# Optimization experiments

Hardware: AMD Instinct MI355X
Metric: run time of the kernel (lower is better)

## Reference

```python
import jax, jax.numpy as jnp
import numpy as np

HEADS = 4
DIM_HEAD = 32
EPS = 1e-5

def _layernorm(x, g, b):
    mu = jnp.mean(x, axis=-1, keepdims=True)
    var = jnp.var(x, axis=-1, keepdims=True)
    return (x - mu) * jax.lax.rsqrt(var + EPS) * g + b

def setup_inputs() -> dict:
    key = jax.random.key(0)
    ks = jax.random.split(key, 8)
    B, C, H, W = 16, 256, 32, 32
    N = H * W
    inner = HEADS * DIM_HEAD  # 128
    s = lambda d: 1.0 / np.sqrt(d)
    return {
        "x": jax.random.normal(ks[0], (B, C, H, W), jnp.float32),
        "pos_embedding": jax.random.normal(ks[1], (1, N, C), jnp.float32),
        "w_qkv": jax.random.normal(ks[2], (C, inner * 3), jnp.float32) * s(C),
        "w_out": jax.random.normal(ks[3], (inner, C), jnp.float32) * s(inner),
        "b_out": jnp.zeros((C,), jnp.float32),
        "w_ff1": jax.random.normal(ks[4], (C, inner), jnp.float32) * s(C),
        "b_ff1": jnp.zeros((inner,), jnp.float32),
        "w_ff2": jax.random.normal(ks[5], (inner, C), jnp.float32) * s(inner),
        "b_ff2": jnp.zeros((C,), jnp.float32),
        "g1": jnp.ones((C,), jnp.float32),
        "beta1": jnp.zeros((C,), jnp.float32),
        "g2": jnp.ones((C,), jnp.float32),
        "beta2": jnp.zeros((C,), jnp.float32),
    }

def reference(x, pos_embedding, w_qkv, w_out, b_out, w_ff1, b_ff1, w_ff2, b_ff2, g1, beta1, g2, beta2):
    b, c, h, w = x.shape
    n = h * w
    tok = jnp.transpose(x.reshape(b, c, n), (0, 2, 1))  # [b, n, c]
    tok = tok + pos_embedding  # (dropout is identity at eval)
    # attention
    qkv = _layernorm(tok, g1, beta1) @ w_qkv  # [b, n, 3*inner]
    qkv = qkv.reshape(b, n, 3, HEADS, DIM_HEAD)
    q, k, v = qkv[:, :, 0], qkv[:, :, 1], qkv[:, :, 2]  # [b, n, h, d]
    scale = DIM_HEAD ** -0.5
    dots = jnp.einsum('bihd,bjhd->bhij', q, k) * scale
    attn = jax.nn.softmax(dots, axis=-1)
    out = jnp.einsum('bhij,bjhd->bihd', attn, v).reshape(b, n, HEADS * DIM_HEAD)
    tok = out @ w_out + b_out + tok
    # ffn
    hdn = jax.nn.gelu(_layernorm(tok, g2, beta2) @ w_ff1 + b_ff1, approximate=False)
    tok = hdn @ w_ff2 + b_ff2 + tok
    return jnp.transpose(tok, (0, 2, 1)).reshape(b, c, h, w)
```

## Files before the change

### kernel.cpp

```cpp
#include <hip/hip_runtime.h>
#include <hip/hip_bf16.h>
#include <math.h>

#define B_     16
#define C_     256
#define N_     1024
#define HEADS_ 4
#define DH_    32
#define INNER_ 128
#define EPS_   1e-5f

typedef __attribute__((ext_vector_type(8))) short bf16x8;
typedef __attribute__((ext_vector_type(4))) float f32x4;

__device__ __forceinline__ ushort f2bf(float f) {
  union { float f; unsigned u; } v; v.f = f;
  unsigned u = v.u;
  return (ushort)((u + 0x7fffu + ((u >> 16) & 1u)) >> 16);
}
__device__ __forceinline__ float bf2f(ushort u) {
  union { unsigned u; float f; } v; v.u = ((unsigned)u) << 16;
  return v.f;
}
__device__ __forceinline__ unsigned cvt_pk_bf16(float lo, float hi) {
  unsigned r;
  asm("v_cvt_pk_bf16_f32 %0, %1, %2" : "=v"(r) : "v"(lo), "v"(hi));
  return r;
}

#define QSCALE_ 0.2550348652979437f

__global__ __launch_bounds__(256) void k_wconv(
    const float* __restrict__ wqkv, const float* __restrict__ wout,
    const float* __restrict__ wff1, const float* __restrict__ wff2,
    ushort* __restrict__ wqkvT, ushort* __restrict__ woutT,
    ushort* __restrict__ wff1T, ushort* __restrict__ wff2T) {
  int i = blockIdx.x * 256 + threadIdx.x;
  if (i < 98304) {
    int k = i / 384, n = i % 384;
    wqkvT[n * 256 + k] = f2bf(wqkv[i]);
    return;
  }
  i -= 98304;
  if (i < 32768) {
    int k = i / 256, n = i % 256;
    woutT[n * 128 + k] = f2bf(wout[i]);
    return;
  }
  i -= 32768;
  if (i < 32768) {
    int k = i / 128, n = i % 128;
    wff1T[n * 256 + k] = f2bf(wff1[i]);
    return;
  }
  i -= 32768;
  {
    int k = i / 256, n = i % 256;
    wff2T[n * 128 + k] = f2bf(wff2[i]);
  }
}

__global__ __launch_bounds__(256) void k_pos_ln(
    const float* __restrict__ x, const float* __restrict__ pos,
    const float* __restrict__ g1, const float* __restrict__ beta1,
    ushort* __restrict__ tokb, ushort* __restrict__ xn) {
  const int b  = blockIdx.x >> 4;
  const int n0 = (blockIdx.x & 15) << 6;
  const int t  = threadIdx.x;
  __shared__ float xs[C_][68];
  {
    const int cq = t >> 4, nq = t & 15;
#pragma unroll
    for (int i = 0; i < 16; ++i) {
      const int c = i * 16 + cq;
      const float4 v = *reinterpret_cast<const float4*>(
          &x[((size_t)b * C_ + c) * N_ + n0 + 4 * nq]);
      *reinterpret_cast<float4*>(&xs[c][4 * nq]) = v;
    }
  }
  __syncthreads();
  const int tl = t >> 2, sub = t & 3, c0 = sub * 64;
  const int n = n0 + tl;
  float v[64];
#pragma unroll
  for (int i = 0; i < 64; ++i) v[i] = xs[c0 + i][tl];
#pragma unroll
  for (int j = 0; j < 16; ++j) {
    const float4 p = *reinterpret_cast<const float4*>(&pos[(size_t)n * C_ + c0 + 4 * j]);
    v[4*j] += p.x; v[4*j+1] += p.y; v[4*j+2] += p.z; v[4*j+3] += p.w;
  }
  float s = 0.f;
#pragma unroll
  for (int i = 0; i < 64; ++i) s += v[i];
  s += __shfl_xor(s, 1); s += __shfl_xor(s, 2);
  const float mu = s * (1.f / C_);
  float sq = 0.f;
#pragma unroll
  for (int i = 0; i < 64; ++i) { const float d = v[i] - mu; sq += d * d; }
  sq += __shfl_xor(sq, 1); sq += __shfl_xor(sq, 2);
  const float rs = rsqrtf(sq * (1.f / C_) + EPS_);
  ushort* tokrow = &tokb[((size_t)b * N_ + n) * C_ + c0];
  ushort* xnrow  = &xn[((size_t)b * N_ + n) * C_ + c0];
#pragma unroll
  for (int j = 0; j < 16; ++j) {
    ushort4 tu;
    tu.x = f2bf(v[4*j]);   tu.y = f2bf(v[4*j+1]);
    tu.z = f2bf(v[4*j+2]); tu.w = f2bf(v[4*j+3]);
    *reinterpret_cast<ushort4*>(&tokrow[4 * j]) = tu;
    const float4 g  = *reinterpret_cast<const float4*>(&g1[c0 + 4 * j]);
    const float4 be = *reinterpret_cast<const float4*>(&beta1[c0 + 4 * j]);
    ushort4 u;
    u.x = f2bf((v[4*j]   - mu) * rs * g.x + be.x);
    u.y = f2bf((v[4*j+1] - mu) * rs * g.y + be.y);
    u.z = f2bf((v[4*j+2] - mu) * rs * g.z + be.z);
    u.w = f2bf((v[4*j+3] - mu) * rs * g.w + be.w);
    *reinterpret_cast<ushort4*>(&xnrow[4 * j]) = u;
  }
}

__global__ __launch_bounds__(256) void k_qkv(
    const ushort* __restrict__ xn, const ushort* __restrict__ wqkvT,
    ushort* __restrict__ qb, ushort* __restrict__ kb, ushort* __restrict__ vtb) {
  const int T0 = blockIdx.x * 32;
  const int w = threadIdx.x >> 6, lane = threadIdx.x & 63;
  const int li = lane & 15, g = lane >> 4;

  bf16x8 Bf[2][8];
#pragma unroll
  for (int nf = 0; nf < 2; ++nf)
#pragma unroll
    for (int ks = 0; ks < 8; ++ks)
      Bf[nf][ks] = *reinterpret_cast<const bf16x8*>(
          &xn[((size_t)(T0 + nf * 16 + li)) * C_ + ks * 32 + 8 * g]);

#pragma unroll
  for (int mf = 0; mf < 6; ++mf) {
    const int chb = w * 96 + mf * 16;
    bf16x8 Af[8];
#pragma unroll
    for (int ks = 0; ks < 8; ++ks)
      Af[ks] = *reinterpret_cast<const bf16x8*>(
          &wqkvT[(size_t)(chb + li) * C_ + ks * 32 + 8 * g]);
#pragma unroll
    for (int nf = 0; nf < 2; ++nf) {
      f32x4 acc = {0.f, 0.f, 0.f, 0.f};
#pragma unroll
      for (int ks = 0; ks < 8; ++ks)
        acc = __builtin_amdgcn_mfma_f32_16x16x32_bf16(Af[ks], Bf[nf][ks], acc, 0, 0, 0);
      const int tokg = T0 + nf * 16 + li;
      const int bb = tokg >> 10, nn = tokg & 1023;
      const int ch0 = chb + 4 * g;
      if (ch0 < 128) {
        const int h = ch0 >> 5, dh = ch0 & 31;
        ushort4 u;
        u.x = f2bf(acc[0] * QSCALE_); u.y = f2bf(acc[1] * QSCALE_);
        u.z = f2bf(acc[2] * QSCALE_); u.w = f2bf(acc[3] * QSCALE_);
        *reinterpret_cast<ushort4*>(&qb[(((size_t)(bb * HEADS_ + h)) * N_ + nn) * DH_ + dh]) = u;
      } else if (ch0 < 256) {
        const int c2 = ch0 - 128, h = c2 >> 5, dh = c2 & 31;
        ushort4 u;
        u.x = f2bf(acc[0]); u.y = f2bf(acc[1]); u.z = f2bf(acc[2]); u.w = f2bf(acc[3]);
        *reinterpret_cast<ushort4*>(&kb[(((size_t)(bb * HEADS_ + h)) * N_ + nn) * DH_ + dh]) = u;
      } else {
        const int c2 = ch0 - 256, h = c2 >> 5, dh = c2 & 31;
        ushort* base = &vtb[(((size_t)(bb * HEADS_ + h)) * DH_ + dh) * N_ + nn];
        base[0] = f2bf(acc[0]); base[N_] = f2bf(acc[1]);
        base[2 * N_] = f2bf(acc[2]); base[3 * N_] = f2bf(acc[3]);
      }
    }
  }
}

__global__ __launch_bounds__(256) void k_attn(
    const ushort* __restrict__ qb, const ushort* __restrict__ kb,
    const ushort* __restrict__ vtb, ushort* __restrict__ ao) {
  const int blk = blockIdx.x;
  const int b   = blk >> 5;
  const int h   = (blk >> 3) & 3;
  const int qt2 = blk & 7;
  const int tid = threadIdx.x;
  const int w = tid >> 6, lane = tid & 63;
  const int qi = lane & 15, g = lane >> 4;

  __shared__ __align__(16) ushort P_lds[4][2][16][80];

  const int bh  = b * HEADS_ + h;
  const int nq0 = qt2 * 128 + w * 32;
  const ushort* Kb = kb  + (size_t)bh * N_ * DH_;
  const ushort* Vt = vtb + (size_t)bh * DH_ * N_;

  bf16x8 qf[2];
#pragma unroll
  for (int G = 0; G < 2; ++G)
    qf[G] = *reinterpret_cast<const bf16x8*>(
        qb + ((size_t)bh * N_ + nq0 + G * 16 + qi) * DH_ + 8 * g);

  f32x4 acc[2][2];
#pragma unroll
  for (int G = 0; G < 2; ++G)
#pragma unroll
    for (int d = 0; d < 2; ++d)
#pragma unroll
      for (int r = 0; r < 4; ++r) acc[G][d][r] = 0.f;
  float m[2] = {-INFINITY, -INFINITY};
  float l[2] = {0.f, 0.f};

  for (int jt = 0; jt < 16; ++jt) {
    const int k0 = jt * 64;
    bf16x8 kf[4];
#pragma unroll
    for (int kt = 0; kt < 4; ++kt)
      kf[kt] = *reinterpret_cast<const bf16x8*>(
          Kb + (size_t)(k0 + kt * 16 + qi) * DH_ + 8 * g);
    bf16x8 vf[2][2];
#pragma unroll
    for (int c = 0; c < 2; ++c)
#pragma unroll
      for (int d = 0; d < 2; ++d)
        vf[c][d] = *reinterpret_cast<const bf16x8*>(
            Vt + (size_t)(d * 16 + qi) * N_ + k0 + c * 32 + 8 * g);

    f32x4 s[2][4];
#pragma unroll
    for (int G = 0; G < 2; ++G)
#pragma unroll
      for (int kt = 0; kt < 4; ++kt) {
        f32x4 z = {0.f, 0.f, 0.f, 0.f};
        s[G][kt] = __builtin_amdgcn_mfma_f32_16x16x32_bf16(kf[kt], qf[G], z, 0, 0, 0);
      }

#pragma unroll
    for (int G = 0; G < 2; ++G) {
      float t0 = fmaxf(fmaxf(s[G][0][0], s[G][0][1]), fmaxf(s[G][0][2], s[G][0][3]));
      float t1 = fmaxf(fmaxf(s[G][1][0], s[G][1][1]), fmaxf(s[G][1][2], s[G][1][3]));
      float t2 = fmaxf(fmaxf(s[G][2][0], s[G][2][1]), fmaxf(s[G][2][2], s[G][2][3]));
      float t3 = fmaxf(fmaxf(s[G][3][0], s[G][3][1]), fmaxf(s[G][3][2], s[G][3][3]));
      float tmax = fmaxf(fmaxf(t0, t1), fmaxf(t2, t3));
      tmax = fmaxf(tmax, __shfl_xor(tmax, 16));
      tmax = fmaxf(tmax, __shfl_xor(tmax, 32));
      if (!__all(tmax <= m[G] + 8.0f)) {
        const float nm = fmaxf(m[G], tmax);
        const float corr = exp2f(m[G] - nm);
#pragma unroll
        for (int d = 0; d < 2; ++d)
#pragma unroll
          for (int r = 0; r < 4; ++r) acc[G][d][r] *= corr;
        l[G] *= corr;
        m[G] = nm;
      }
      float psum = 0.f;
#pragma unroll
      for (int kt = 0; kt < 4; ++kt) {
        const float p0 = exp2f(s[G][kt][0] - m[G]);
        const float p1 = exp2f(s[G][kt][1] - m[G]);
        const float p2 = exp2f(s[G][kt][2] - m[G]);
        const float p3 = exp2f(s[G][kt][3] - m[G]);
        psum += (p0 + p1) + (p2 + p3);
        uint2 dw;
        dw.x = cvt_pk_bf16(p0, p1);
        dw.y = cvt_pk_bf16(p2, p3);
        *reinterpret_cast<uint2*>(&P_lds[w][G][qi][kt * 16 + 4 * g]) = dw;
      }
      l[G] += psum;
    }

#pragma unroll
    for (int c = 0; c < 2; ++c) {
      const bf16x8 pf0 = *reinterpret_cast<const bf16x8*>(&P_lds[w][0][qi][c * 32 + 8 * g]);
      const bf16x8 pf1 = *reinterpret_cast<const bf16x8*>(&P_lds[w][1][qi][c * 32 + 8 * g]);
#pragma unroll
      for (int d = 0; d < 2; ++d) {
        acc[0][d] = __builtin_amdgcn_mfma_f32_16x16x32_bf16(vf[c][d], pf0, acc[0][d], 0, 0, 0);
        acc[1][d] = __builtin_amdgcn_mfma_f32_16x16x32_bf16(vf[c][d], pf1, acc[1][d], 0, 0, 0);
      }
    }
  }

#pragma unroll
  for (int G = 0; G < 2; ++G) {
    float lg = l[G];
    lg += __shfl_xor(lg, 16);
    lg += __shfl_xor(lg, 32);
    const float inv = 1.f / lg;
    const int n = nq0 + G * 16 + qi;
#pragma unroll
    for (int d = 0; d < 2; ++d) {
      ushort4 u;
      u.x = f2bf(acc[G][d][0] * inv);
      u.y = f2bf(acc[G][d][1] * inv);
      u.z = f2bf(acc[G][d][2] * inv);
      u.w = f2bf(acc[G][d][3] * inv);
      *reinterpret_cast<ushort4*>(
          &ao[((size_t)b * N_ + n) * INNER_ + h * DH_ + d * 16 + 4 * g]) = u;
    }
  }
}

__global__ __launch_bounds__(256) void k_mlp(
    const ushort* __restrict__ ao, const ushort* __restrict__ tokb,
    const ushort* __restrict__ woutT, const float* __restrict__ b_out,
    const ushort* __restrict__ wff1T, const float* __restrict__ b_ff1,
    const ushort* __restrict__ wff2T, const float* __restrict__ b_ff2,
    const float* __restrict__ g2, const float* __restrict__ beta2,
    float* __restrict__ out) {
  const int T0 = blockIdx.x * 32;
  const int bb = T0 >> 10;
  const int nb = T0 & 1023;
  const int tid = threadIdx.x;
  const int w = tid >> 6, lane = tid & 63, li = lane & 15, g = lane >> 4;

  __shared__ float  t2s[32][260];
  __shared__ ushort xn2[32][264];
  __shared__ ushort hsb[32][136];

  {
    bf16x8 Af[2][4];
#pragma unroll
    for (int mf = 0; mf < 2; ++mf)
#pragma unroll
      for (int ks = 0; ks < 4; ++ks)
        Af[mf][ks] = *reinterpret_cast<const bf16x8*>(
            &ao[((size_t)(T0 + mf * 16 + li)) * INNER_ + ks * 32 + 8 * g]);
#pragma unroll
    for (int nf = 0; nf < 4; ++nf) {
      const int n = w * 64 + nf * 16;
      bf16x8 Bf[4];
#pragma unroll
      for (int ks = 0; ks < 4; ++ks)
        Bf[ks] = *reinterpret_cast<const bf16x8*>(
            &woutT[(size_t)(n + li) * INNER_ + ks * 32 + 8 * g]);
#pragma unroll
      for (int mf = 0; mf < 2; ++mf) {
        f32x4 acc = {0.f, 0.f, 0.f, 0.f};
#pragma unroll
        for (int ks = 0; ks < 4; ++ks)
          acc = __builtin_amdgcn_mfma_f32_16x16x32_bf16(Af[mf][ks], Bf[ks], acc, 0, 0, 0);
        const int nch = n + li;
        const int tl0 = mf * 16 + 4 * g;
        const float bo = b_out[nch];
#pragma unroll
        for (int r = 0; r < 4; ++r)
          t2s[tl0 + r][nch] =
              acc[r] + bo + bf2f(tokb[((size_t)(T0 + tl0 + r)) * C_ + nch]);
      }
    }
  }
  __syncthreads();

  {
    const int tl = tid >> 3, c0 = (tid & 7) * 32;
    float v[32];
#pragma unroll
    for (int j = 0; j < 8; ++j) {
      const float4 t4 = *reinterpret_cast<const float4*>(&t2s[tl][c0 + 4 * j]);
      v[4*j] = t4.x; v[4*j+1] = t4.y; v[4*j+2] = t4.z; v[4*j+3] = t4.w;
    }
    float s = 0.f;
#pragma unroll
    for (int i = 0; i < 32; ++i) s += v[i];
    s += __shfl_xor(s, 1); s += __shfl_xor(s, 2); s += __shfl_xor(s, 4);
    const float mu = s * (1.f / C_);
    float sq = 0.f;
#pragma unroll
    for (int i = 0; i < 32; ++i) { const float d = v[i] - mu; sq += d * d; }
    sq += __shfl_xor(sq, 1); sq += __shfl_xor(sq, 2); sq += __shfl_xor(sq, 4);
    const float rs = rsqrtf(sq * (1.f / C_) + EPS_);
#pragma unroll
    for (int j = 0; j < 8; ++j) {
      const float4 gg = *reinterpret_cast<const float4*>(&g2[c0 + 4 * j]);
      const float4 be = *reinterpret_cast<const float4*>(&beta2[c0 + 4 * j]);
      ushort4 u;
      u.x = f2bf((v[4*j]   - mu) * rs * gg.x + be.x);
      u.y = f2bf((v[4*j+1] - mu) * rs * gg.y + be.y);
      u.z = f2bf((v[4*j+2] - mu) * rs * gg.z + be.z);
      u.w = f2bf((v[4*j+3] - mu) * rs * gg.w + be.w);
      *reinterpret_cast<ushort4*>(&xn2[tl][c0 + 4 * j]) = u;
    }
  }
  __syncthreads();

  {
    bf16x8 Af[2][8];
#pragma unroll
    for (int mf = 0; mf < 2; ++mf)
#pragma unroll
      for (int ks = 0; ks < 8; ++ks)
        Af[mf][ks] = *reinterpret_cast<const bf16x8*>(&xn2[mf * 16 + li][ks * 32 + 8 * g]);
#pragma unroll
    for (int nf = 0; nf < 2; ++nf) {
      const int n = w * 32 + nf * 16;
      bf16x8 Bf[8];
#pragma unroll
      for (int ks = 0; ks < 8; ++ks)
        Bf[ks] = *reinterpret_cast<const bf16x8*>(
            &wff1T[(size_t)(n + li) * C_ + ks * 32 + 8 * g]);
#pragma unroll
      for (int mf = 0; mf < 2; ++mf) {
        f32x4 acc = {0.f, 0.f, 0.f, 0.f};
#pragma unroll
        for (int ks = 0; ks < 8; ++ks)
          acc = __builtin_amdgcn_mfma_f32_16x16x32_bf16(Af[mf][ks], Bf[ks], acc, 0, 0, 0);
        const int nch = n + li;
        const int tl0 = mf * 16 + 4 * g;
        const float bf1 = b_ff1[nch];
#pragma unroll
        for (int r = 0; r < 4; ++r) {
          float hv = acc[r] + bf1;
          hv = 0.5f * hv * (1.f + erff(hv * 0.70710678118654752f));
          hsb[tl0 + r][nch] = f2bf(hv);
        }
      }
    }
  }
  __syncthreads();

  {
    bf16x8 Af[2][4];
#pragma unroll
    for (int mf = 0; mf < 2; ++mf)
#pragma unroll
      for (int ks = 0; ks < 4; ++ks)
        Af[mf][ks] = *reinterpret_cast<const bf16x8*>(&hsb[mf * 16 + li][ks * 32 + 8 * g]);
#pragma unroll
    for (int nf = 0; nf < 4; ++nf) {
      const int n = w * 64 + nf * 16;
      bf16x8 Bf[4];
#pragma unroll
      for (int ks = 0; ks < 4; ++ks)
        Bf[ks] = *reinterpret_cast<const bf16x8*>(
            &wff2T[(size_t)(n + li) * INNER_ + ks * 32 + 8 * g]);
#pragma unroll
      for (int mf = 0; mf < 2; ++mf) {
        f32x4 acc = {0.f, 0.f, 0.f, 0.f};
#pragma unroll
        for (int ks = 0; ks < 4; ++ks)
          acc = __builtin_amdgcn_mfma_f32_16x16x32_bf16(Af[mf][ks], Bf[ks], acc, 0, 0, 0);
        const int nch = n + li;
        const int tl0 = mf * 16 + 4 * g;
        const float bo = b_ff2[nch];
        float4 o;
        o.x = acc[0] + bo + t2s[tl0 + 0][nch];
        o.y = acc[1] + bo + t2s[tl0 + 1][nch];
        o.z = acc[2] + bo + t2s[tl0 + 2][nch];
        o.w = acc[3] + bo + t2s[tl0 + 3][nch];
        *reinterpret_cast<float4*>(
            &out[((size_t)bb * C_ + nch) * N_ + nb + tl0]) = o;
      }
    }
  }
}

extern "C" void kernel_launch(void* const* d_in, const int* in_sizes, int n_in,
                              void* d_out, int out_size, void* d_ws, size_t ws_size,
                              hipStream_t stream) {
  const float* x     = (const float*)d_in[0];
  const float* pos   = (const float*)d_in[1];
  const float* w_qkv = (const float*)d_in[2];
  const float* w_out = (const float*)d_in[3];
  const float* b_out = (const float*)d_in[4];
  const float* w_ff1 = (const float*)d_in[5];
  const float* b_ff1 = (const float*)d_in[6];
  const float* w_ff2 = (const float*)d_in[7];
  const float* b_ff2 = (const float*)d_in[8];
  const float* g1    = (const float*)d_in[9];
  const float* beta1 = (const float*)d_in[10];
  const float* g2    = (const float*)d_in[11];
  const float* beta2 = (const float*)d_in[12];
  float* out = (float*)d_out;

  ushort* tokb  = (ushort*)d_ws;
  ushort* xn    = tokb + 4194304;
  ushort* ao    = xn + 4194304;
  ushort* qb    = ao + 2097152;
  ushort* kb    = qb + 2097152;
  ushort* vtb   = kb + 2097152;
  ushort* wqkvT = vtb + 2097152;
  ushort* woutT = wqkvT + 98304;
  ushort* wff1T = woutT + 32768;
  ushort* wff2T = wff1T + 32768;

  k_wconv<<<768, 256, 0, stream>>>(w_qkv, w_out, w_ff1, w_ff2,
                                   wqkvT, woutT, wff1T, wff2T);
  k_pos_ln<<<256, 256, 0, stream>>>(x, pos, g1, beta1, tokb, xn);
  k_qkv<<<512, 256, 0, stream>>>(xn, wqkvT, qb, kb, vtb);
  k_attn<<<512, 256, 0, stream>>>(qb, kb, vtb, ao);
  k_mlp<<<512, 256, 0, stream>>>(ao, tokb, woutT, b_out, wff1T, b_ff1,
                                 wff2T, b_ff2, g2, beta2, out);
}
```

Measured before the change: 176.3 us.

## Fuse pos-add/LayerNorm with QKV projection, keeping normalized tile in LDS

Merges the positional-add plus LayerNorm kernel with the QKV projection GEMM. Each block normalizes 64 tokens and stages the bf16 result in LDS, aliased over the transpose buffer through a union. The MFMA GEMM then reads that tile from LDS instead of a global xn buffer. This drops one kernel launch and the 8 MB round trip of xn through HBM, but the grid shrinks from 512 to 256 blocks for the GEMM part and adds extra barriers.

```diff
diff --git a/kernel.cpp b/kernel.cpp
--- a/kernel.cpp
+++ b/kernel.cpp
@@ -60,14 +60,21 @@
   }
 }
 
-__global__ __launch_bounds__(256) void k_pos_ln(
+union KFusedSmem {
+  float  xs[C_][68];
+  ushort xnl[64][264];
+};
+
+__global__ __launch_bounds__(256) void k_fused(
     const float* __restrict__ x, const float* __restrict__ pos,
     const float* __restrict__ g1, const float* __restrict__ beta1,
-    ushort* __restrict__ tokb, ushort* __restrict__ xn) {
+    const ushort* __restrict__ wqkvT, ushort* __restrict__ tokb,
+    ushort* __restrict__ qb, ushort* __restrict__ kb, ushort* __restrict__ vtb) {
   const int b  = blockIdx.x >> 4;
   const int n0 = (blockIdx.x & 15) << 6;
   const int t  = threadIdx.x;
-  __shared__ float xs[C_][68];
+  __shared__ KFusedSmem u;
+
   {
     const int cq = t >> 4, nq = t & 15;
 #pragma unroll
@@ -75,97 +82,96 @@
       const int c = i * 16 + cq;
       const float4 v = *reinterpret_cast<const float4*>(
           &x[((size_t)b * C_ + c) * N_ + n0 + 4 * nq]);
-      *reinterpret_cast<float4*>(&xs[c][4 * nq]) = v;
+      *reinterpret_cast<float4*>(&u.xs[c][4 * nq]) = v;
     }
   }
   __syncthreads();
-  const int tl = t >> 2, sub = t & 3, c0 = sub * 64;
-  const int n = n0 + tl;
-  float v[64];
-#pragma unroll
-  for (int i = 0; i < 64; ++i) v[i] = xs[c0 + i][tl];
-#pragma unroll
-  for (int j = 0; j < 16; ++j) {
-    const float4 p = *reinterpret_cast<const float4*>(&pos[(size_t)n * C_ + c0 + 4 * j]);
-    v[4*j] += p.x; v[4*j+1] += p.y; v[4*j+2] += p.z; v[4*j+3] += p.w;
-  }
-  float s = 0.f;
-#pragma unroll
-  for (int i = 0; i < 64; ++i) s += v[i];
-  s += __shfl_xor(s, 1); s += __shfl_xor(s, 2);
-  const float mu = s * (1.f / C_);
-  float sq = 0.f;
-#pragma unroll
-  for (int i = 0; i < 64; ++i) { const float d = v[i] - mu; sq += d * d; }
-  sq += __shfl_xor(sq, 1); sq += __shfl_xor(sq, 2);
-  const float rs = rsqrtf(sq * (1.f / C_) + EPS_);
-  ushort* tokrow = &tokb[((size_t)b * N_ + n) * C_ + c0];
-  ushort* xnrow  = &xn[((size_t)b * N_ + n) * C_ + c0];
-#pragma unroll
-  for (int j = 0; j < 16; ++j) {
-    ushort4 tu;
-    tu.x = f2bf(v[4*j]);   tu.y = f2bf(v[4*j+1]);
-    tu.z = f2bf(v[4*j+2]); tu.w = f2bf(v[4*j+3]);
-    *reinterpret_cast<ushort4*>(&tokrow[4 * j]) = tu;
-    const float4 g  = *reinterpret_cast<const float4*>(&g1[c0 + 4 * j]);
-    const float4 be = *reinterpret_cast<const float4*>(&beta1[c0 + 4 * j]);
-    ushort4 u;
-    u.x = f2bf((v[4*j]   - mu) * rs * g.x + be.x);
-    u.y = f2bf((v[4*j+1] - mu) * rs * g.y + be.y);
-    u.z = f2bf((v[4*j+2] - mu) * rs * g.z + be.z);
-    u.w = f2bf((v[4*j+3] - mu) * rs * g.w + be.w);
-    *reinterpret_cast<ushort4*>(&xnrow[4 * j]) = u;
-  }
-}
-
-__global__ __launch_bounds__(256) void k_qkv(
-    const ushort* __restrict__ xn, const ushort* __restrict__ wqkvT,
-    ushort* __restrict__ qb, ushort* __restrict__ kb, ushort* __restrict__ vtb) {
-  const int T0 = blockIdx.x * 32;
-  const int w = threadIdx.x >> 6, lane = threadIdx.x & 63;
-  const int li = lane & 15, g = lane >> 4;
-
-  bf16x8 Bf[2][8];
-#pragma unroll
-  for (int nf = 0; nf < 2; ++nf)
-#pragma unroll
-    for (int ks = 0; ks < 8; ++ks)
-      Bf[nf][ks] = *reinterpret_cast<const bf16x8*>(
-          &xn[((size_t)(T0 + nf * 16 + li)) * C_ + ks * 32 + 8 * g]);
-
-#pragma unroll
-  for (int mf = 0; mf < 6; ++mf) {
-    const int chb = w * 96 + mf * 16;
-    bf16x8 Af[8];
-#pragma unroll
-    for (int ks = 0; ks < 8; ++ks)
-      Af[ks] = *reinterpret_cast<const bf16x8*>(
-          &wqkvT[(size_t)(chb + li) * C_ + ks * 32 + 8 * g]);
-#pragma unroll
-    for (int nf = 0; nf < 2; ++nf) {
-      f32x4 acc = {0.f, 0.f, 0.f, 0.f};
+
+  {
+    const int tl = t >> 2, sub = t & 3, c0 = sub * 64;
+    const int n = n0 + tl;
+    float v[64];
+#pragma unroll
+    for (int i = 0; i < 64; ++i) v[i] = u.xs[c0 + i][tl];
+#pragma unroll
+    for (int j = 0; j < 16; ++j) {
+      const float4 p = *reinterpret_cast<const float4*>(&pos[(size_t)n * C_ + c0 + 4 * j]);
+      v[4*j] += p.x; v[4*j+1] += p.y; v[4*j+2] += p.z; v[4*j+3] += p.w;
+    }
+    float s = 0.f;
+#pragma unroll
+    for (int i = 0; i < 64; ++i) s += v[i];
+    s += __shfl_xor(s, 1); s += __shfl_xor(s, 2);
+    const float mu = s * (1.f / C_);
+    float sq = 0.f;
+#pragma unroll
+    for (int i = 0; i < 64; ++i) { const float d = v[i] - mu; sq += d * d; }
+    sq += __shfl_xor(sq, 1); sq += __shfl_xor(sq, 2);
+    const float rs = rsqrtf(sq * (1.f / C_) + EPS_);
+
+    ushort* tokrow = &tokb[((size_t)b * N_ + n) * C_ + c0];
+    ushort xn_local[64];
+#pragma unroll
+    for (int j = 0; j < 16; ++j) {
+      ushort4 tu;
+      tu.x = f2bf(v[4*j]);   tu.y = f2bf(v[4*j+1]);
+      tu.z = f2bf(v[4*j+2]); tu.w = f2bf(v[4*j+3]);
+      *reinterpret_cast<ushort4*>(&tokrow[4 * j]) = tu;
+      const float4 g  = *reinterpret_cast<const float4*>(&g1[c0 + 4 * j]);
+      const float4 be = *reinterpret_cast<const float4*>(&beta1[c0 + 4 * j]);
+      xn_local[4*j]   = f2bf((v[4*j]   - mu) * rs * g.x + be.x);
+      xn_local[4*j+1] = f2bf((v[4*j+1] - mu) * rs * g.y + be.y);
+      xn_local[4*j+2] = f2bf((v[4*j+2] - mu) * rs * g.z + be.z);
+      xn_local[4*j+3] = f2bf((v[4*j+3] - mu) * rs * g.w + be.w);
+    }
+    __syncthreads();
+#pragma unroll
+    for (int j = 0; j < 16; ++j)
+      *reinterpret_cast<ushort4*>(&u.xnl[tl][c0 + 4 * j]) =
+          *reinterpret_cast<ushort4*>(&xn_local[4 * j]);
+  }
+  __syncthreads();
+
+  {
+    const int w = t >> 6, lane = t & 63;
+    const int li = lane & 15, g = lane >> 4;
+#pragma unroll
+    for (int mf = 0; mf < 6; ++mf) {
+      const int chb = w * 96 + mf * 16;
+      bf16x8 Af[8];
 #pragma unroll
       for (int ks = 0; ks < 8; ++ks)
-        acc = __builtin_amdgcn_mfma_f32_16x16x32_bf16(Af[ks], Bf[nf][ks], acc, 0, 0, 0);
-      const int tokg = T0 + nf * 16 + li;
-      const int bb = tokg >> 10, nn = tokg & 1023;
-      const int ch0 = chb + 4 * g;
-      if (ch0 < 128) {
-        const int h = ch0 >> 5, dh = ch0 & 31;
-        ushort4 u;
-        u.x = f2bf(acc[0] * QSCALE_); u.y = f2bf(acc[1] * QSCALE_);
-        u.z = f2bf(acc[2] * QSCALE_); u.w = f2bf(acc[3] * QSCALE_);
-        *reinterpret_cast<ushort4*>(&qb[(((size_t)(bb * HEADS_ + h)) * N_ + nn) * DH_ + dh]) = u;
-      } else if (ch0 < 256) {
-        const int c2 = ch0 - 128, h = c2 >> 5, dh = c2 & 31;
-        ushort4 u;
-        u.x = f2bf(acc[0]); u.y = f2bf(acc[1]); u.z = f2bf(acc[2]); u.w = f2bf(acc[3]);
-        *reinterpret_cast<ushort4*>(&kb[(((size_t)(bb * HEADS_ + h)) * N_ + nn) * DH_ + dh]) = u;
-      } else {
-        const int c2 = ch0 - 256, h = c2 >> 5, dh = c2 & 31;
-        ushort* base = &vtb[(((size_t)(bb * HEADS_ + h)) * DH_ + dh) * N_ + nn];
-        base[0] = f2bf(acc[0]); base[N_] = f2bf(acc[1]);
-        base[2 * N_] = f2bf(acc[2]); base[3 * N_] = f2bf(acc[3]);
+        Af[ks] = *reinterpret_cast<const bf16x8*>(
+            &wqkvT[(size_t)(chb + li) * C_ + ks * 32 + 8 * g]);
+#pragma unroll
+      for (int nf = 0; nf < 4; ++nf) {
+        bf16x8 Bf[8];
+#pragma unroll
+        for (int ks = 0; ks < 8; ++ks)
+          Bf[ks] = *reinterpret_cast<const bf16x8*>(&u.xnl[nf * 16 + li][ks * 32 + 8 * g]);
+        f32x4 acc = {0.f, 0.f, 0.f, 0.f};
+#pragma unroll
+        for (int ks = 0; ks < 8; ++ks)
+          acc = __builtin_amdgcn_mfma_f32_16x16x32_bf16(Af[ks], Bf[ks], acc, 0, 0, 0);
+        const int nn = n0 + nf * 16 + li;
+        const int ch0 = chb + 4 * g;
+        if (ch0 < 128) {
+          const int h = ch0 >> 5, dh = ch0 & 31;
+          ushort4 uq;
+          uq.x = f2bf(acc[0] * QSCALE_); uq.y = f2bf(acc[1] * QSCALE_);
+          uq.z = f2bf(acc[2] * QSCALE_); uq.w = f2bf(acc[3] * QSCALE_);
+          *reinterpret_cast<ushort4*>(&qb[(((size_t)(b * HEADS_ + h)) * N_ + nn) * DH_ + dh]) = uq;
+        } else if (ch0 < 256) {
+          const int c2 = ch0 - 128, h = c2 >> 5, dh = c2 & 31;
+          ushort4 uk;
+          uk.x = f2bf(acc[0]); uk.y = f2bf(acc[1]); uk.z = f2bf(acc[2]); uk.w = f2bf(acc[3]);
+          *reinterpret_cast<ushort4*>(&kb[(((size_t)(b * HEADS_ + h)) * N_ + nn) * DH_ + dh]) = uk;
+        } else {
+          const int c2 = ch0 - 256, h = c2 >> 5, dh = c2 & 31;
+          ushort* base = &vtb[(((size_t)(b * HEADS_ + h)) * DH_ + dh) * N_ + nn];
+          base[0] = f2bf(acc[0]); base[N_] = f2bf(acc[1]);
+          base[2 * N_] = f2bf(acc[2]); base[3 * N_] = f2bf(acc[3]);
+        }
       }
     }
   }
@@ -285,13 +291,13 @@
     const int n = nq0 + G * 16 + qi;
 #pragma unroll
     for (int d = 0; d < 2; ++d) {
-      ushort4 u;
-      u.x = f2bf(acc[G][d][0] * inv);
-      u.y = f2bf(acc[G][d][1] * inv);
-      u.z = f2bf(acc[G][d][2] * inv);
-      u.w = f2bf(acc[G][d][3] * inv);
+      ushort4 uo;
+      uo.x = f2bf(acc[G][d][0] * inv);
+      uo.y = f2bf(acc[G][d][1] * inv);
+      uo.z = f2bf(acc[G][d][2] * inv);
+      uo.w = f2bf(acc[G][d][3] * inv);
       *reinterpret_cast<ushort4*>(
-          &ao[((size_t)b * N_ + n) * INNER_ + h * DH_ + d * 16 + 4 * g]) = u;
+          &ao[((size_t)b * N_ + n) * INNER_ + h * DH_ + d * 16 + 4 * g]) = uo;
     }
   }
 }
@@ -469,8 +475,7 @@
   float* out = (float*)d_out;
 
   ushort* tokb  = (ushort*)d_ws;
-  ushort* xn    = tokb + 4194304;
-  ushort* ao    = xn + 4194304;
+  ushort* ao    = tokb + 4194304;
   ushort* qb    = ao + 2097152;
   ushort* kb    = qb + 2097152;
   ushort* vtb   = kb + 2097152;
@@ -481,8 +486,7 @@
 
   k_wconv<<<768, 256, 0, stream>>>(w_qkv, w_out, w_ff1, w_ff2,
                                    wqkvT, woutT, wff1T, wff2T);
-  k_pos_ln<<<256, 256, 0, stream>>>(x, pos, g1, beta1, tokb, xn);
-  k_qkv<<<512, 256, 0, stream>>>(xn, wqkvT, qb, kb, vtb);
+  k_fused<<<256, 256, 0, stream>>>(x, pos, g1, beta1, wqkvT, tokb, qb, kb, vtb);
   k_attn<<<512, 256, 0, stream>>>(qb, kb, vtb, ao);
   k_mlp<<<512, 256, 0, stream>>>(ao, tokb, woutT, b_out, wff1T, b_ff1,
                                  wff2T, b_ff2, g2, beta2, out);
```

Measured after the change: 167.4 us. 1.05x faster.
